# Kernel tuning notes

Hardware: AMD Instinct MI355X
Metric: run time of the kernel (lower is better)

Reference implementation:

```python
import jax, jax.numpy as jnp
import numpy as np

NUM_CLASSES = 10
ALPHA = 0.25
GAMMA = 2.0
BETA = 1.0
EPS = 1e-7


def _corners(centers, dims, yaws):
    # centers [N,2], dims [N,2] (l,w), yaws [N] -> corners [N,4,2]
    half = dims * 0.5
    base = jnp.array([[1., 1.], [-1., 1.], [-1., -1.], [1., -1.]], dtype=centers.dtype)
    base = base[None, :, :] * half[:, None, :]  # [N,4,2]
    c, s = jnp.cos(yaws), jnp.sin(yaws)
    x = base[..., 0] * c[:, None] - base[..., 1] * s[:, None]
    y = base[..., 0] * s[:, None] + base[..., 1] * c[:, None]
    corners = jnp.stack([x, y], axis=-1) + centers[:, None, :]
    return corners[:, jnp.array([3, 2, 1, 0]), :]  # reorder as in torch code


def _cross(u, v):
    return u[..., 0] * v[..., 1] - u[..., 1] * v[..., 0]


def _signed_area(q):  # q [...,4,2]
    return 0.5 * jnp.sum(_cross(q, jnp.roll(q, -1, axis=-2)), axis=-1)


def _pts_in_quad(pts, quad, sgn):
    # pts [N,P,2] inside convex quad [N,4,2]; sgn = orientation sign of quad [N]
    a = quad
    e = jnp.roll(quad, -1, axis=-2) - a  # [N,4,2]
    d = pts[:, :, None, :] - a[:, None, :, :]  # [N,P,4,2]
    cr = e[:, None, :, 0] * d[..., 1] - e[:, None, :, 1] * d[..., 0]  # [N,P,4]
    return jnp.all(cr * sgn[:, None, None] >= -1e-9, axis=-1)


def _rotated_iou(cA, cB):
    # Exact convex-quad intersection IoU (replaces the per-box Shapely loop).
    N = cA.shape[0]
    sgnA = jnp.sign(_signed_area(cA))
    sgnB = jnp.sign(_signed_area(cB))
    vA_in_B = _pts_in_quad(cA, cB, sgnB)  # [N,4]
    vB_in_A = _pts_in_quad(cB, cA, sgnA)  # [N,4]
    # all 4x4 edge-edge intersections
    a1 = cA; a2 = jnp.roll(cA, -1, axis=1)
    b1 = cB; b2 = jnp.roll(cB, -1, axis=1)
    da = (a2 - a1)[:, :, None, :]  # [N,4,1,2]
    db = (b2 - b1)[:, None, :, :]  # [N,1,4,2]
    dp = b1[:, None, :, :] - a1[:, :, None, :]  # [N,4,4,2]
    den = _cross(da, db)  # [N,4,4]
    den_safe = jnp.where(jnp.abs(den) < 1e-12, 1.0, den)
    t = _cross(dp, db) / den_safe
    s = _cross(dp, da) / den_safe
    val_x = (jnp.abs(den) > 1e-12) & (t >= 0) & (t <= 1) & (s >= 0) & (s <= 1)
    xpts = a1[:, :, None, :] + t[..., None] * da  # [N,4,4,2]
    # up to 24 candidate vertices of the convex intersection polygon
    pts = jnp.concatenate([cA, cB, xpts.reshape(N, 16, 2)], axis=1)  # [N,24,2]
    valid = jnp.concatenate([vA_in_B, vB_in_A, val_x.reshape(N, 16)], axis=1)
    pts = jnp.where(valid[..., None], pts, 0.0)
    nv = valid.sum(axis=1)
    cent = pts.sum(axis=1) / jnp.maximum(nv, 1)[:, None]
    ang = jnp.arctan2(pts[..., 1] - cent[:, None, 1], pts[..., 0] - cent[:, None, 0])
    key = jnp.where(valid, ang, 1e9)
    order = jnp.argsort(key, axis=1)
    ps = jnp.take_along_axis(pts, order[..., None], axis=1)
    vs = jnp.take_along_axis(valid, order, axis=1)
    ps = jnp.where(vs[..., None], ps, ps[:, :1, :])  # pad with first valid vertex
    inter = 0.5 * jnp.abs(jnp.sum(_cross(ps, jnp.roll(ps, -1, axis=1)), axis=1))
    inter = jnp.where(nv >= 3, inter, 0.0)
    areaA = jnp.abs(_signed_area(cA))
    areaB = jnp.abs(_signed_area(cB))
    union = areaA + areaB - inter
    return jnp.where(union > 1e-7, inter / union, 0.0)


def _sl1(p, t):
    d = jnp.abs(p - t)
    return jnp.where(d < BETA, 0.5 * d * d / BETA, d - 0.5 * BETA)


def setup_inputs() -> dict:
    key = jax.random.key(0)
    ks = jax.random.split(key, 7)
    B, C, H, W = 8, NUM_CLASSES, 256, 256
    cls_pred = jax.random.normal(ks[0], (B, C, H, W), dtype=jnp.float32)
    reg_pred = jax.random.uniform(ks[1], (B, 9, H, W), dtype=jnp.float32)
    iou_pred = jax.random.normal(ks[2], (B, 1, H, W), dtype=jnp.float32)
    cls_targets = jax.random.randint(ks[3], (B, H, W), 0, C, dtype=jnp.int32)
    reg_targets = jax.random.uniform(ks[4], (B, 9, H, W), dtype=jnp.float32)
    reg_weights = jax.random.randint(ks[5], (B, H, W), 0, 2).astype(jnp.float32)
    iou_targets = jax.random.uniform(ks[6], (B, 1, H, W), dtype=jnp.float32)
    return {"cls_pred": cls_pred, "reg_pred": reg_pred, "iou_pred": iou_pred,
            "cls_targets": cls_targets, "reg_targets": reg_targets,
            "reg_weights": reg_weights, "iou_targets": iou_targets}


def reference(cls_pred, reg_pred, iou_pred, cls_targets, reg_targets, reg_weights, iou_targets):
    B, C, H, W = cls_pred.shape
    N = B * H * W
    clsf = jnp.transpose(cls_pred, (0, 2, 3, 1)).reshape(N, C)
    regf = jnp.transpose(reg_pred, (0, 2, 3, 1)).reshape(N, 9)
    regt = jnp.transpose(reg_targets, (0, 2, 3, 1)).reshape(N, 9)
    iouf = jnp.transpose(iou_pred, (0, 2, 3, 1)).reshape(N)
    iout = iou_targets.reshape(N)
    ct = cls_targets.reshape(N)
    w = reg_weights.reshape(N)
    pos = (w > 0).astype(clsf.dtype)
    num_pos = jnp.maximum(pos.sum(), 1.0)
    # focal classification loss
    valid = ct >= 0
    p = jax.nn.softmax(clsf, axis=1)
    tl = jnp.clip(ct, 0, C - 1)
    pt = jnp.clip(jnp.take_along_axis(p, tl[:, None], axis=1)[:, 0], EPS, 1.0 - EPS)
    alpha_t = jnp.where(ct > 0, ALPHA, 1.0 - ALPHA)
    fl = -alpha_t * (1.0 - pt) ** GAMMA * jnp.log(pt)
    cls_loss = jnp.sum(jnp.where(valid, fl, 0.0)) / num_pos
    cen_p, dim_p, yaw_p = regf[:, :2], regf[:, 3:5], regf[:, 6]
    cen_t, dim_t, yaw_t = regt[:, :2], regt[:, 3:5], regt[:, 6]
    cp = _corners(cen_p, dim_p, yaw_p)
    ctg = _corners(cen_t, dim_t, yaw_t)
    iou = jax.lax.stop_gradient(_rotated_iou(cp, ctg))
    d2 = jnp.sum((cen_p - cen_t) ** 2, axis=-1)
    allc = jnp.concatenate([cp, ctg], axis=1)  # [N,8,2]
    c2 = jnp.maximum(jnp.sum((allc.max(axis=1) - allc.min(axis=1)) ** 2, axis=-1), EPS)
    loss_bev = 1.0 - iou + d2 / c2
    at_p = jnp.arctan(dim_p[:, 1] / jnp.maximum(dim_p[:, 0], EPS))
    at_t = jnp.arctan(dim_t[:, 1] / jnp.maximum(dim_t[:, 0], EPS))
    v = (4.0 / np.pi ** 2) * (at_p - at_t) ** 2
    alpha_c = jax.lax.stop_gradient(v / (1.0 - iou + v + EPS))
    loss_bev = loss_bev + alpha_c * v
    bev_loss = jnp.sum(loss_bev * pos) / num_pos
    # smooth-L1 terms: z (ch 2), h (ch 5), vel (ch 7:9)
    z_loss = jnp.sum(_sl1(regf[:, 2], regt[:, 2]) * pos) / num_pos
    h_loss = jnp.sum(_sl1(regf[:, 5], regt[:, 5]) * pos) / num_pos
    vel_loss = jnp.sum(_sl1(regf[:, 7:9], regt[:, 7:9]).sum(axis=-1) * pos) / num_pos
    # BCE-with-logits IoU head loss
    x, y = iouf, iout
    bce = jnp.maximum(x, 0.0) - x * y + jnp.log1p(jnp.exp(-jnp.abs(x)))
    iou_loss = jnp.sum(bce * pos) / num_pos
    return jnp.stack([cls_loss, bev_loss, z_loss, h_loss, vel_loss, iou_loss])
```

## Files before the change

### kernel.cpp

```cpp
#include <hip/hip_runtime.h>
#include <cstdint>
#include <cstddef>

#define B_ 8
#define C_ 10
#define HW_ 65536
#define NPIX_ (B_ * HW_)

__device__ __forceinline__ float sl1f(float p, float t) {
    float d = fabsf(p - t);
    return (d < 1.0f) ? 0.5f * d * d : d - 0.5f;
}

__global__ __launch_bounds__(256) void bev_loss_main(
    const float* __restrict__ cls_pred, const float* __restrict__ reg_pred,
    const float* __restrict__ iou_pred, const int* __restrict__ cls_tg,
    const float* __restrict__ reg_tg, const float* __restrict__ reg_w,
    const float* __restrict__ iou_tg, double* __restrict__ part)
{
    double acc0 = 0, acc1 = 0, acc2 = 0, acc3 = 0, acc4 = 0, acc5 = 0, acc6 = 0;
    int stride = gridDim.x * blockDim.x;
    for (int n = blockIdx.x * blockDim.x + threadIdx.x; n < NPIX_; n += stride) {
        int b  = n >> 16;
        int hw = n & 65535;

        {
            const float* cp = cls_pred + (size_t)b * C_ * HW_ + hw;
            float lg[C_];
            #pragma unroll
            for (int c = 0; c < C_; c++) lg[c] = cp[(size_t)c * HW_];
            int ct = cls_tg[n];
            float m = lg[0];
            #pragma unroll
            for (int c = 1; c < C_; c++) m = fmaxf(m, lg[c]);
            float se = 0.f;
            #pragma unroll
            for (int c = 0; c < C_; c++) se += expf(lg[c] - m);
            int tl = ct < 0 ? 0 : (ct > C_ - 1 ? C_ - 1 : ct);
            float pt = expf(lg[tl] - m) / se;
            pt = fminf(fmaxf(pt, 1e-7f), 1.0f - 1e-7f);
            float alpha_t = (ct > 0) ? 0.25f : 0.75f;
            float omp = 1.0f - pt;
            float fl = -alpha_t * omp * omp * logf(pt);
            float vmask = (ct >= 0) ? 1.0f : 0.0f;
            acc0 += (double)(fl * vmask);
        }

        float P[9], T[9];
        {
            const float* rp = reg_pred + (size_t)b * 9 * HW_ + hw;
            const float* rt = reg_tg  + (size_t)b * 9 * HW_ + hw;
            #pragma unroll
            for (int k = 0; k < 9; k++) { P[k] = rp[(size_t)k * HW_]; T[k] = rt[(size_t)k * HW_]; }
        }
        float w = reg_w[n];
        float pos = (w > 0.f) ? 1.f : 0.f;

        float Ax[4], Ay[4], Bx[4], By[4];
        {
            const float sbx[4] = { 1.f, -1.f, -1.f, 1.f };
            const float sby[4] = { -1.f, -1.f, 1.f, 1.f };
            float hx = 0.5f * P[3], hy = 0.5f * P[4];
            float ss, cc; __sincosf(P[6], &ss, &cc);
            #pragma unroll
            for (int i = 0; i < 4; i++) {
                float px = sbx[i] * hx, py = sby[i] * hy;
                Ax[i] = px * cc - py * ss + P[0];
                Ay[i] = px * ss + py * cc + P[1];
            }
            float hx2 = 0.5f * T[3], hy2 = 0.5f * T[4];
            float ss2, cc2; __sincosf(T[6], &ss2, &cc2);
            #pragma unroll
            for (int i = 0; i < 4; i++) {
                float px = sbx[i] * hx2, py = sby[i] * hy2;
                Bx[i] = px * cc2 - py * ss2 + T[0];
                By[i] = px * ss2 + py * cc2 + T[1];
            }
        }

        float sa = 0.f, sb = 0.f;
        #pragma unroll
        for (int i = 0; i < 4; i++) {
            int j = (i + 1) & 3;
            sa += Ax[i] * Ay[j] - Ay[i] * Ax[j];
            sb += Bx[i] * By[j] - By[i] * Bx[j];
        }
        sa *= 0.5f; sb *= 0.5f;
        float sgnA = (sa > 0.f) ? 1.f : ((sa < 0.f) ? -1.f : 0.f);
        float sgnB = (sb > 0.f) ? 1.f : ((sb < 0.f) ? -1.f : 0.f);

        float dB[4][4], dA[4][4];
        #pragma unroll
        for (int j = 0; j < 4; j++) {
            int j1 = (j + 1) & 3;
            float ex = Bx[j1] - Bx[j], ey = By[j1] - By[j];
            #pragma unroll
            for (int i = 0; i < 4; i++)
                dB[j][i] = sgnB * (ex * (Ay[i] - By[j]) - ey * (Ax[i] - Bx[j]));
        }
        #pragma unroll
        for (int j = 0; j < 4; j++) {
            int j1 = (j + 1) & 3;
            float ex = Ax[j1] - Ax[j], ey = Ay[j1] - Ay[j];
            #pragma unroll
            for (int i = 0; i < 4; i++)
                dA[j][i] = sgnA * (ex * (By[i] - Ay[j]) - ey * (Bx[i] - Ax[j]));
        }

        float S = 0.f;
        #pragma unroll
        for (int i = 0; i < 4; i++) {
            int i1 = (i + 1) & 3;
            float t0 = 0.f, t1 = 1.f;
            #pragma unroll
            for (int j = 0; j < 4; j++) {
                float d0 = dB[j][i], d1 = dB[j][i1];
                float den = d1 - d0;
                float t = __fdividef(-d0, den);
                if (den > 0.f)       t0 = fmaxf(t0, t);
                else if (den < 0.f)  t1 = fminf(t1, t);
                else if (d0 < 0.f)   t0 = 2.f;
            }
            S += (Ax[i] * Ay[i1] - Ay[i] * Ax[i1]) * fmaxf(t1 - t0, 0.f);
        }
        #pragma unroll
        for (int i = 0; i < 4; i++) {
            int i1 = (i + 1) & 3;
            float t0 = 0.f, t1 = 1.f;
            #pragma unroll
            for (int j = 0; j < 4; j++) {
                float d0 = dA[j][i], d1 = dA[j][i1];
                float den = d1 - d0;
                float t = __fdividef(-d0, den);
                if (den > 0.f)       t0 = fmaxf(t0, t);
                else if (den < 0.f)  t1 = fminf(t1, t);
                else if (d0 < 0.f)   t0 = 2.f;
            }
            S += (Bx[i] * By[i1] - By[i] * Bx[i1]) * fmaxf(t1 - t0, 0.f);
        }
        float inter = 0.5f * fabsf(S);

        float areaA = fabsf(sa), areaB = fabsf(sb);
        float uni = areaA + areaB - inter;
        float iou = (uni > 1e-7f) ? inter / uni : 0.f;

        float ddx = P[0] - T[0], ddy = P[1] - T[1];
        float d2 = ddx * ddx + ddy * ddy;
        float mnx = Ax[0], mxx = Ax[0], mny = Ay[0], mxy = Ay[0];
        #pragma unroll
        for (int i = 1; i < 4; i++) {
            mnx = fminf(mnx, Ax[i]); mxx = fmaxf(mxx, Ax[i]);
            mny = fminf(mny, Ay[i]); mxy = fmaxf(mxy, Ay[i]);
        }
        #pragma unroll
        for (int i = 0; i < 4; i++) {
            mnx = fminf(mnx, Bx[i]); mxx = fmaxf(mxx, Bx[i]);
            mny = fminf(mny, By[i]); mxy = fmaxf(mxy, By[i]);
        }
        float ex_ = mxx - mnx, ey_ = mxy - mny;
        float c2 = fmaxf(ex_ * ex_ + ey_ * ey_, 1e-7f);

        float atp = atanf(P[4] / fmaxf(P[3], 1e-7f));
        float att = atanf(T[4] / fmaxf(T[3], 1e-7f));
        float dv = atp - att;
        float v = 0.4052847345693511f * dv * dv;
        float alpha_c = v / (1.0f - iou + v + 1e-7f);
        float lbev = 1.0f - iou + d2 / c2 + alpha_c * v;
        acc1 += (double)(lbev * pos);

        acc2 += (double)(sl1f(P[2], T[2]) * pos);
        acc3 += (double)(sl1f(P[5], T[5]) * pos);
        acc4 += (double)((sl1f(P[7], T[7]) + sl1f(P[8], T[8])) * pos);

        {
            float x = iou_pred[n], y = iou_tg[n];
            float bce = fmaxf(x, 0.f) - x * y + log1pf(expf(-fabsf(x)));
            acc5 += (double)(bce * pos);
        }
        acc6 += (double)pos;
    }

    __shared__ double red[4][7];
    double a[7] = { acc0, acc1, acc2, acc3, acc4, acc5, acc6 };
    int lane = threadIdx.x & 63;
    int wv = threadIdx.x >> 6;
    #pragma unroll
    for (int k = 0; k < 7; k++) {
        double s = a[k];
        for (int off = 32; off > 0; off >>= 1) s += __shfl_down(s, off, 64);
        if (lane == 0) red[wv][k] = s;
    }
    __syncthreads();
    if (threadIdx.x == 0) {
        #pragma unroll
        for (int k = 0; k < 7; k++)
            part[(size_t)blockIdx.x * 7 + k] = red[0][k] + red[1][k] + red[2][k] + red[3][k];
    }
}

__global__ void bev_loss_fin(const double* __restrict__ part, float* __restrict__ out, int nb) {
    int l = threadIdx.x;
    double s[7] = { 0, 0, 0, 0, 0, 0, 0 };
    for (int i = l; i < nb; i += 64) {
        #pragma unroll
        for (int k = 0; k < 7; k++) s[k] += part[(size_t)i * 7 + k];
    }
    #pragma unroll
    for (int k = 0; k < 7; k++) {
        for (int off = 32; off > 0; off >>= 1) s[k] += __shfl_down(s[k], off, 64);
    }
    if (l == 0) {
        double npos = fmax(s[6], 1.0);
        #pragma unroll
        for (int k = 0; k < 6; k++) out[k] = (float)(s[k] / npos);
    }
}

extern "C" void kernel_launch(void* const* d_in, const int* in_sizes, int n_in,
                              void* d_out, int out_size, void* d_ws, size_t ws_size,
                              hipStream_t stream) {
    const float* cls_pred = (const float*)d_in[0];
    const float* reg_pred = (const float*)d_in[1];
    const float* iou_pred = (const float*)d_in[2];
    const int*   cls_tg   = (const int*)d_in[3];
    const float* reg_tg   = (const float*)d_in[4];
    const float* reg_w    = (const float*)d_in[5];
    const float* iou_tg   = (const float*)d_in[6];
    float* out = (float*)d_out;
    double* part = (double*)d_ws;

    int nb = 2048;
    size_t need = (size_t)nb * 7 * sizeof(double);
    if (ws_size < need) {
        nb = (int)(ws_size / (7 * sizeof(double)));
        if (nb < 1) nb = 1;
    }

    bev_loss_main<<<nb, 256, 0, stream>>>(cls_pred, reg_pred, iou_pred, cls_tg,
                                          reg_tg, reg_w, iou_tg, part);
    bev_loss_fin<<<1, 64, 0, stream>>>(part, out, nb);
}
```

Before: 41.51 us.

## Process two pixels per thread with float2 loads and fast-math intrinsics

Replaces the grid-stride loop with a fixed grid of 1024 blocks where each thread handles exactly two adjacent pixels, loaded as float2/int2 vectors. Per-pixel math moves into a helper and swaps expf/logf/divides for __expf/__logf/__fdividef. The intent is wider memory transactions, more loads in flight per thread, and cheaper transcendentals. It drops the workspace-size check and hardcodes coverage of exactly NPIX pixels, and the fast intrinsics are less accurate.

```diff
diff --git a/kernel.cpp b/kernel.cpp
--- a/kernel.cpp
+++ b/kernel.cpp
@@ -10,6 +10,151 @@
 __device__ __forceinline__ float sl1f(float p, float t) {
     float d = fabsf(p - t);
     return (d < 1.0f) ? 0.5f * d * d : d - 0.5f;
+}
+
+__device__ __forceinline__ void pixel_loss(
+    const float lg[C_], int ct, const float P[9], const float T[9],
+    float w, float xiou, float yiou, float o[7])
+{
+    float m = lg[0];
+    #pragma unroll
+    for (int c = 1; c < C_; c++) m = fmaxf(m, lg[c]);
+    float se = 0.f;
+    float ex[C_];
+    #pragma unroll
+    for (int c = 0; c < C_; c++) { ex[c] = __expf(lg[c] - m); se += ex[c]; }
+    int tl = ct < 0 ? 0 : (ct > C_ - 1 ? C_ - 1 : ct);
+    float et = 0.f;
+    #pragma unroll
+    for (int c = 0; c < C_; c++) et = (c == tl) ? ex[c] : et;
+    float pt = __fdividef(et, se);
+    pt = fminf(fmaxf(pt, 1e-7f), 1.0f - 1e-7f);
+    float alpha_t = (ct > 0) ? 0.25f : 0.75f;
+    float omp = 1.0f - pt;
+    float fl = -alpha_t * omp * omp * __logf(pt);
+    o[0] = (ct >= 0) ? fl : 0.0f;
+
+    float pos = (w > 0.f) ? 1.f : 0.f;
+
+    float Ax[4], Ay[4], Bx[4], By[4];
+    {
+        const float sbx[4] = { 1.f, -1.f, -1.f, 1.f };
+        const float sby[4] = { -1.f, -1.f, 1.f, 1.f };
+        float hx = 0.5f * P[3], hy = 0.5f * P[4];
+        float ss, cc; __sincosf(P[6], &ss, &cc);
+        #pragma unroll
+        for (int i = 0; i < 4; i++) {
+            float px = sbx[i] * hx, py = sby[i] * hy;
+            Ax[i] = px * cc - py * ss + P[0];
+            Ay[i] = px * ss + py * cc + P[1];
+        }
+        float hx2 = 0.5f * T[3], hy2 = 0.5f * T[4];
+        float ss2, cc2; __sincosf(T[6], &ss2, &cc2);
+        #pragma unroll
+        for (int i = 0; i < 4; i++) {
+            float px = sbx[i] * hx2, py = sby[i] * hy2;
+            Bx[i] = px * cc2 - py * ss2 + T[0];
+            By[i] = px * ss2 + py * cc2 + T[1];
+        }
+    }
+
+    float sa = 0.f, sb = 0.f;
+    #pragma unroll
+    for (int i = 0; i < 4; i++) {
+        int j = (i + 1) & 3;
+        sa += Ax[i] * Ay[j] - Ay[i] * Ax[j];
+        sb += Bx[i] * By[j] - By[i] * Bx[j];
+    }
+    sa *= 0.5f; sb *= 0.5f;
+    float sgnA = (sa > 0.f) ? 1.f : ((sa < 0.f) ? -1.f : 0.f);
+    float sgnB = (sb > 0.f) ? 1.f : ((sb < 0.f) ? -1.f : 0.f);
+
+    float dB[4][4], dA[4][4];
+    #pragma unroll
+    for (int j = 0; j < 4; j++) {
+        int j1 = (j + 1) & 3;
+        float ex_ = Bx[j1] - Bx[j], ey_ = By[j1] - By[j];
+        #pragma unroll
+        for (int i = 0; i < 4; i++)
+            dB[j][i] = sgnB * (ex_ * (Ay[i] - By[j]) - ey_ * (Ax[i] - Bx[j]));
+    }
+    #pragma unroll
+    for (int j = 0; j < 4; j++) {
+        int j1 = (j + 1) & 3;
+        float ex_ = Ax[j1] - Ax[j], ey_ = Ay[j1] - Ay[j];
+        #pragma unroll
+        for (int i = 0; i < 4; i++)
+            dA[j][i] = sgnA * (ex_ * (By[i] - Ay[j]) - ey_ * (Bx[i] - Ax[j]));
+    }
+
+    float S = 0.f;
+    #pragma unroll
+    for (int i = 0; i < 4; i++) {
+        int i1 = (i + 1) & 3;
+        float t0 = 0.f, t1 = 1.f;
+        #pragma unroll
+        for (int j = 0; j < 4; j++) {
+            float d0 = dB[j][i], d1 = dB[j][i1];
+            float den = d1 - d0;
+            float t = __fdividef(-d0, den);
+            if (den > 0.f)       t0 = fmaxf(t0, t);
+            else if (den < 0.f)  t1 = fminf(t1, t);
+            else if (d0 < 0.f)   t0 = 2.f;
+        }
+        S += (Ax[i] * Ay[i1] - Ay[i] * Ax[i1]) * fmaxf(t1 - t0, 0.f);
+    }
+    #pragma unroll
+    for (int i = 0; i < 4; i++) {
+        int i1 = (i + 1) & 3;
+        float t0 = 0.f, t1 = 1.f;
+        #pragma unroll
+        for (int j = 0; j < 4; j++) {
+            float d0 = dA[j][i], d1 = dA[j][i1];
+            float den = d1 - d0;
+            float t = __fdividef(-d0, den);
+            if (den > 0.f)       t0 = fmaxf(t0, t);
+            else if (den < 0.f)  t1 = fminf(t1, t);
+            else if (d0 < 0.f)   t0 = 2.f;
+        }
+        S += (Bx[i] * By[i1] - By[i] * Bx[i1]) * fmaxf(t1 - t0, 0.f);
+    }
+    float inter = 0.5f * fabsf(S);
+
+    float areaA = fabsf(sa), areaB = fabsf(sb);
+    float uni = areaA + areaB - inter;
+    float iou = (uni > 1e-7f) ? __fdividef(inter, uni) : 0.f;
+
+    float ddx = P[0] - T[0], ddy = P[1] - T[1];
+    float d2 = ddx * ddx + ddy * ddy;
+    float mnx = Ax[0], mxx = Ax[0], mny = Ay[0], mxy = Ay[0];
+    #pragma unroll
+    for (int i = 1; i < 4; i++) {
+        mnx = fminf(mnx, Ax[i]); mxx = fmaxf(mxx, Ax[i]);
+        mny = fminf(mny, Ay[i]); mxy = fmaxf(mxy, Ay[i]);
+    }
+    #pragma unroll
+    for (int i = 0; i < 4; i++) {
+        mnx = fminf(mnx, Bx[i]); mxx = fmaxf(mxx, Bx[i]);
+        mny = fminf(mny, By[i]); mxy = fmaxf(mxy, By[i]);
+    }
+    float exd = mxx - mnx, eyd = mxy - mny;
+    float c2 = fmaxf(exd * exd + eyd * eyd, 1e-7f);
+
+    float atp = atanf(__fdividef(P[4], fmaxf(P[3], 1e-7f)));
+    float att = atanf(__fdividef(T[4], fmaxf(T[3], 1e-7f)));
+    float dv = atp - att;
+    float v = 0.4052847345693511f * dv * dv;
+    float alpha_c = __fdividef(v, 1.0f - iou + v + 1e-7f);
+    float lbev = 1.0f - iou + __fdividef(d2, c2) + alpha_c * v;
+    o[1] = lbev * pos;
+
+    o[2] = sl1f(P[2], T[2]) * pos;
+    o[3] = sl1f(P[5], T[5]) * pos;
+    o[4] = (sl1f(P[7], T[7]) + sl1f(P[8], T[8])) * pos;
+
+    float bce = fmaxf(xiou, 0.f) - xiou * yiou + __logf(1.0f + __expf(-fabsf(xiou)));
+    o[5] = bce * pos;
+    o[6] = pos;
 }
 
 __global__ __launch_bounds__(256) void bev_loss_main(
@@ -18,175 +163,57 @@
     const float* __restrict__ reg_tg, const float* __restrict__ reg_w,
     const float* __restrict__ iou_tg, double* __restrict__ part)
 {
-    double acc0 = 0, acc1 = 0, acc2 = 0, acc3 = 0, acc4 = 0, acc5 = 0, acc6 = 0;
-    int stride = gridDim.x * blockDim.x;
-    for (int n = blockIdx.x * blockDim.x + threadIdx.x; n < NPIX_; n += stride) {
-        int b  = n >> 16;
-        int hw = n & 65535;
-
-        {
-            const float* cp = cls_pred + (size_t)b * C_ * HW_ + hw;
-            float lg[C_];
-            #pragma unroll
-            for (int c = 0; c < C_; c++) lg[c] = cp[(size_t)c * HW_];
-            int ct = cls_tg[n];
-            float m = lg[0];
-            #pragma unroll
-            for (int c = 1; c < C_; c++) m = fmaxf(m, lg[c]);
-            float se = 0.f;
-            #pragma unroll
-            for (int c = 0; c < C_; c++) se += expf(lg[c] - m);
-            int tl = ct < 0 ? 0 : (ct > C_ - 1 ? C_ - 1 : ct);
-            float pt = expf(lg[tl] - m) / se;
-            pt = fminf(fmaxf(pt, 1e-7f), 1.0f - 1e-7f);
-            float alpha_t = (ct > 0) ? 0.25f : 0.75f;
-            float omp = 1.0f - pt;
-            float fl = -alpha_t * omp * omp * logf(pt);
-            float vmask = (ct >= 0) ? 1.0f : 0.0f;
-            acc0 += (double)(fl * vmask);
-        }
-
-        float P[9], T[9];
-        {
-            const float* rp = reg_pred + (size_t)b * 9 * HW_ + hw;
-            const float* rt = reg_tg  + (size_t)b * 9 * HW_ + hw;
-            #pragma unroll
-            for (int k = 0; k < 9; k++) { P[k] = rp[(size_t)k * HW_]; T[k] = rt[(size_t)k * HW_]; }
-        }
-        float w = reg_w[n];
-        float pos = (w > 0.f) ? 1.f : 0.f;
-
-        float Ax[4], Ay[4], Bx[4], By[4];
-        {
-            const float sbx[4] = { 1.f, -1.f, -1.f, 1.f };
-            const float sby[4] = { -1.f, -1.f, 1.f, 1.f };
-            float hx = 0.5f * P[3], hy = 0.5f * P[4];
-            float ss, cc; __sincosf(P[6], &ss, &cc);
-            #pragma unroll
-            for (int i = 0; i < 4; i++) {
-                float px = sbx[i] * hx, py = sby[i] * hy;
-                Ax[i] = px * cc - py * ss + P[0];
-                Ay[i] = px * ss + py * cc + P[1];
-            }
-            float hx2 = 0.5f * T[3], hy2 = 0.5f * T[4];
-            float ss2, cc2; __sincosf(T[6], &ss2, &cc2);
-            #pragma unroll
-            for (int i = 0; i < 4; i++) {
-                float px = sbx[i] * hx2, py = sby[i] * hy2;
-                Bx[i] = px * cc2 - py * ss2 + T[0];
-                By[i] = px * ss2 + py * cc2 + T[1];
-            }
-        }
-
-        float sa = 0.f, sb = 0.f;
-        #pragma unroll
-        for (int i = 0; i < 4; i++) {
-            int j = (i + 1) & 3;
-            sa += Ax[i] * Ay[j] - Ay[i] * Ax[j];
-            sb += Bx[i] * By[j] - By[i] * Bx[j];
-        }
-        sa *= 0.5f; sb *= 0.5f;
-        float sgnA = (sa > 0.f) ? 1.f : ((sa < 0.f) ? -1.f : 0.f);
-        float sgnB = (sb > 0.f) ? 1.f : ((sb < 0.f) ? -1.f : 0.f);
-
-        float dB[4][4], dA[4][4];
-        #pragma unroll
-        for (int j = 0; j < 4; j++) {
-            int j1 = (j + 1) & 3;
-            float ex = Bx[j1] - Bx[j], ey = By[j1] - By[j];
-            #pragma unroll
-            for (int i = 0; i < 4; i++)
-                dB[j][i] = sgnB * (ex * (Ay[i] - By[j]) - ey * (Ax[i] - Bx[j]));
-        }
-        #pragma unroll
-        for (int j = 0; j < 4; j++) {
-            int j1 = (j + 1) & 3;
-            float ex = Ax[j1] - Ax[j], ey = Ay[j1] - Ay[j];
-            #pragma unroll
-            for (int i = 0; i < 4; i++)
-                dA[j][i] = sgnA * (ex * (By[i] - Ay[j]) - ey * (Bx[i] - Ax[j]));
-        }
-
-        float S = 0.f;
-        #pragma unroll
-        for (int i = 0; i < 4; i++) {
-            int i1 = (i + 1) & 3;
-            float t0 = 0.f, t1 = 1.f;
-            #pragma unroll
-            for (int j = 0; j < 4; j++) {
-                float d0 = dB[j][i], d1 = dB[j][i1];
-                float den = d1 - d0;
-                float t = __fdividef(-d0, den);
-                if (den > 0.f)       t0 = fmaxf(t0, t);
-                else if (den < 0.f)  t1 = fminf(t1, t);
-                else if (d0 < 0.f)   t0 = 2.f;
-            }
-            S += (Ax[i] * Ay[i1] - Ay[i] * Ax[i1]) * fmaxf(t1 - t0, 0.f);
-        }
-        #pragma unroll
-        for (int i = 0; i < 4; i++) {
-            int i1 = (i + 1) & 3;
-            float t0 = 0.f, t1 = 1.f;
-            #pragma unroll
-            for (int j = 0; j < 4; j++) {
-                float d0 = dA[j][i], d1 = dA[j][i1];
-                float den = d1 - d0;
-                float t = __fdividef(-d0, den);
-                if (den > 0.f)       t0 = fmaxf(t0, t);
-                else if (den < 0.f)  t1 = fminf(t1, t);
-                else if (d0 < 0.f)   t0 = 2.f;
-            }
-            S += (Bx[i] * By[i1] - By[i] * Bx[i1]) * fmaxf(t1 - t0, 0.f);
-        }
-        float inter = 0.5f * fabsf(S);
-
-        float areaA = fabsf(sa), areaB = fabsf(sb);
-        float uni = areaA + areaB - inter;
-        float iou = (uni > 1e-7f) ? inter / uni : 0.f;
-
-        float ddx = P[0] - T[0], ddy = P[1] - T[1];
-        float d2 = ddx * ddx + ddy * ddy;
-        float mnx = Ax[0], mxx = Ax[0], mny = Ay[0], mxy = Ay[0];
-        #pragma unroll
-        for (int i = 1; i < 4; i++) {
-            mnx = fminf(mnx, Ax[i]); mxx = fmaxf(mxx, Ax[i]);
-            mny = fminf(mny, Ay[i]); mxy = fmaxf(mxy, Ay[i]);
-        }
-        #pragma unroll
-        for (int i = 0; i < 4; i++) {
-            mnx = fminf(mnx, Bx[i]); mxx = fmaxf(mxx, Bx[i]);
-            mny = fminf(mny, By[i]); mxy = fmaxf(mxy, By[i]);
-        }
-        float ex_ = mxx - mnx, ey_ = mxy - mny;
-        float c2 = fmaxf(ex_ * ex_ + ey_ * ey_, 1e-7f);
-
-        float atp = atanf(P[4] / fmaxf(P[3], 1e-7f));
-        float att = atanf(T[4] / fmaxf(T[3], 1e-7f));
-        float dv = atp - att;
-        float v = 0.4052847345693511f * dv * dv;
-        float alpha_c = v / (1.0f - iou + v + 1e-7f);
-        float lbev = 1.0f - iou + d2 / c2 + alpha_c * v;
-        acc1 += (double)(lbev * pos);
-
-        acc2 += (double)(sl1f(P[2], T[2]) * pos);
-        acc3 += (double)(sl1f(P[5], T[5]) * pos);
-        acc4 += (double)((sl1f(P[7], T[7]) + sl1f(P[8], T[8])) * pos);
-
-        {
-            float x = iou_pred[n], y = iou_tg[n];
-            float bce = fmaxf(x, 0.f) - x * y + log1pf(expf(-fabsf(x)));
-            acc5 += (double)(bce * pos);
-        }
-        acc6 += (double)pos;
+    int t  = blockIdx.x * blockDim.x + threadIdx.x;
+    int n0 = t << 1;
+    int b  = n0 >> 16;
+    int hw = n0 & 65535;
+
+    float2 lg2[C_];
+    {
+        const float* cp = cls_pred + (size_t)b * C_ * HW_ + hw;
+        #pragma unroll
+        for (int c = 0; c < C_; c++)
+            lg2[c] = *reinterpret_cast<const float2*>(cp + (size_t)c * HW_);
+    }
+    float2 P2[9], T2[9];
+    {
+        const float* rp = reg_pred + (size_t)b * 9 * HW_ + hw;
+        const float* rt = reg_tg  + (size_t)b * 9 * HW_ + hw;
+        #pragma unroll
+        for (int k = 0; k < 9; k++) {
+            P2[k] = *reinterpret_cast<const float2*>(rp + (size_t)k * HW_);
+            T2[k] = *reinterpret_cast<const float2*>(rt + (size_t)k * HW_);
+        }
+    }
+    int2   ct2 = *reinterpret_cast<const int2*>(cls_tg + n0);
+    float2 w2  = *reinterpret_cast<const float2*>(reg_w + n0);
+    float2 x2  = *reinterpret_cast<const float2*>(iou_pred + n0);
+    float2 y2  = *reinterpret_cast<const float2*>(iou_tg + n0);
+
+    float o0[7], o1[7];
+    {
+        float lg[C_], P[9], T[9];
+        #pragma unroll
+        for (int c = 0; c < C_; c++) lg[c] = lg2[c].x;
+        #pragma unroll
+        for (int k = 0; k < 9; k++) { P[k] = P2[k].x; T[k] = T2[k].x; }
+        pixel_loss(lg, ct2.x, P, T, w2.x, x2.x, y2.x, o0);
+    }
+    {
+        float lg[C_], P[9], T[9];
+        #pragma unroll
+        for (int c = 0; c < C_; c++) lg[c] = lg2[c].y;
+        #pragma unroll
+        for (int k = 0; k < 9; k++) { P[k] = P2[k].y; T[k] = T2[k].y; }
+        pixel_loss(lg, ct2.y, P, T, w2.y, x2.y, y2.y, o1);
     }
 
     __shared__ double red[4][7];
-    double a[7] = { acc0, acc1, acc2, acc3, acc4, acc5, acc6 };
     int lane = threadIdx.x & 63;
-    int wv = threadIdx.x >> 6;
+    int wv   = threadIdx.x >> 6;
     #pragma unroll
     for (int k = 0; k < 7; k++) {
-        double s = a[k];
+        double s = (double)o0[k] + (double)o1[k];
         for (int off = 32; off > 0; off >>= 1) s += __shfl_down(s, off, 64);
         if (lane == 0) red[wv][k] = s;
     }
@@ -229,13 +256,7 @@
     float* out = (float*)d_out;
     double* part = (double*)d_ws;
 
-    int nb = 2048;
-    size_t need = (size_t)nb * 7 * sizeof(double);
-    if (ws_size < need) {
-        nb = (int)(ws_size / (7 * sizeof(double)));
-        if (nb < 1) nb = 1;
-    }
-
+    const int nb = 1024;
     bev_loss_main<<<nb, 256, 0, stream>>>(cls_pred, reg_pred, iou_pred, cls_tg,
                                           reg_tg, reg_w, iou_tg, part);
     bev_loss_fin<<<1, 64, 0, stream>>>(part, out, nb);
```

Measured after the change: 37.77 us. 9.0% less time.
